# Kernel tuning notes

Measured on AMD Instinct MI355X. Metric: run time of the kernel, lower is better.

The kernel has to match this reference:

```python
import jax, jax.numpy as jnp
import numpy as np

QUERY_LEVELS = jnp.array([300, 500, 900, 1500], dtype=jnp.int32)
MAX_K = 1500
NUM_BOUNDARIES = 3
MAX_OBJECTS = 1500
SCALE = MAX_OBJECTS / NUM_BOUNDARIES * 0.3  # 150.0


def _layernorm(x, g, b, eps=1e-5):
    m = jnp.mean(x, axis=-1, keepdims=True)
    v = jnp.var(x, axis=-1, keepdims=True)
    return (x - m) * jax.lax.rsqrt(v + eps) * g + b


def setup_inputs() -> dict:
    key = jax.random.key(0)
    ks = jax.random.split(key, 14)
    B, C, H, W = 8, 256, 100, 100
    s = 0.02
    return {
        "density_feature": jax.random.normal(ks[0], (B, C, H, W), jnp.float32),
        "encoder_features": jax.random.normal(ks[1], (B, C, H, W), jnp.float32),
        # input_norm (LayerNorm over 2*C)
        "ln_in_g": jnp.ones((2 * C,), jnp.float32),
        "ln_in_b": jnp.zeros((2 * C,), jnp.float32),
        # fc_boundary: Linear(2C->C), Linear(C->3)
        "fcb_w1": jax.random.normal(ks[2], (C, 2 * C), jnp.float32) * s,
        "fcb_b1": jnp.zeros((C,), jnp.float32),
        "fcb_w2": jax.random.normal(ks[3], (NUM_BOUNDARIES, C), jnp.float32) * s,
        "fcb_b2": jnp.full((NUM_BOUNDARIES,), -3.0, jnp.float32),
        "cr_ln_g": jnp.ones((C,), jnp.float32),
        "cr_ln_b": jnp.zeros((C,), jnp.float32),
        "cr_w1": jax.random.normal(ks[4], (C, C), jnp.float32) * s,
        "cr_b1": jnp.zeros((C,), jnp.float32),
        "cr_w2": jax.random.normal(ks[5], (1, C), jnp.float32) * s,
        "cr_b2": jnp.full((1,), 4.0, jnp.float32),
        # channel attention 1x1 convs: C->C//16->C
        "ca_w1": jax.random.normal(ks[6], (C // 16, C), jnp.float32) * s,
        "ca_b1": jnp.zeros((C // 16,), jnp.float32),
        "ca_w2": jax.random.normal(ks[7], (C, C // 16), jnp.float32) * s,
        "ca_b2": jnp.zeros((C,), jnp.float32),
        # spatial attention 7x7 conv, 2->1, no bias
        "sa_w": jax.random.normal(ks[8], (1, 2, 7, 7), jnp.float32) * s,
        # spatial_weight_conv 1x1, C->1
        "sw_w": jax.random.normal(ks[9], (1, C), jnp.float32) * s,
        "sw_b": jnp.zeros((1,), jnp.float32),
    }


def reference(density_feature, encoder_features, ln_in_g, ln_in_b,
              fcb_w1, fcb_b1, fcb_w2, fcb_b2,
              cr_ln_g, cr_ln_b, cr_w1, cr_b1, cr_w2, cr_b2,
              ca_w1, ca_b1, ca_w2, ca_b2, sa_w, sw_w, sw_b):
    B, C, H, W = density_feature.shape
    df = jnp.clip(density_feature, -5.0, 5.0)
    ef = jnp.clip(encoder_features, -5.0, 5.0)

    # ---- boundary prediction from density feature ----
    feat_avg = jnp.mean(df, axis=(2, 3))            # [B, C]
    feat_max = jnp.max(df, axis=(2, 3))             # [B, C]
    gfeat = jnp.concatenate([feat_avg, feat_max], axis=1)  # [B, 2C]
    gfeat = _layernorm(gfeat, ln_in_g, ln_in_b)
    h = jax.nn.relu(gfeat @ fcb_w1.T + fcb_b1)
    raw_boundaries = h @ fcb_w2.T + fcb_b2           # [B, 3]
    # cumulative: b_i = sum_{j<=i} (softplus(raw_j)*SCALE + 5)
    boundaries = jnp.cumsum(jax.nn.softplus(raw_boundaries) * SCALE + 5.0, axis=1)

    cr = _layernorm(feat_avg, cr_ln_g, cr_ln_b)
    cr = jax.nn.relu(cr @ cr_w1.T + cr_b1)
    pred_count = jax.nn.softplus(cr @ cr_w2.T + cr_b2)[:, 0]  # [B]

    # ---- num_queries via boundary comparison (eval: N_eval = pred_count) ----
    level = ((pred_count > boundaries[:, 0]).astype(jnp.int32)
             + (pred_count > boundaries[:, 1]).astype(jnp.int32)
             + (pred_count > boundaries[:, 2]).astype(jnp.int32))
    num_queries = QUERY_LEVELS[level]

    # ---- CBAM channel attention ----
    x = ef
    gap = jnp.mean(x, axis=(2, 3))                   # [B, C]
    ca = jax.nn.relu(gap @ ca_w1.T + ca_b1)
    ca = jax.nn.sigmoid(ca @ ca_w2.T + ca_b2)        # [B, C]
    x = x * ca[:, :, None, None]

    # ---- CBAM spatial attention ----
    sa_avg = jnp.mean(x, axis=1, keepdims=True)      # [B,1,H,W]
    sa_max = jnp.max(x, axis=1, keepdims=True)
    sa = jnp.concatenate([sa_avg, sa_max], axis=1)   # [B,2,H,W]
    sa = jax.lax.conv_general_dilated(sa, sa_w, (1, 1), [(3, 3), (3, 3)],
                                      dimension_numbers=("NCHW", "OIHW", "NCHW"))
    x = x * jax.nn.sigmoid(sa)

    # ---- spatial weight map + topk reference points ----
    wmap = jax.nn.sigmoid(jnp.einsum("bchw,oc->bohw", x, sw_w) + sw_b[None, :, None, None])
    spatial_weight_map = wmap.reshape(B, 1, H * W)
    weight_flat = wmap.reshape(B, H * W)
    actual_k = min(H * W, MAX_K)
    _, topk_ind = jax.lax.top_k(weight_flat, actual_k)   # [B, k]
    topk_y = ((topk_ind // W).astype(jnp.float32) + 0.5) / H
    topk_x = ((topk_ind % W).astype(jnp.float32) + 0.5) / W
    ref_points = jnp.stack([topk_x, topk_y], axis=-1)    # [B,k,2]
    ref_points = jnp.concatenate([ref_points, jnp.full_like(ref_points, 0.05)], axis=-1)
    if actual_k < MAX_K:
        pad = jnp.zeros((B, MAX_K - actual_k, 4), ref_points.dtype)
        ref_points = jnp.concatenate([ref_points, pad], axis=1)

    return (boundaries, raw_boundaries, pred_count, num_queries,
            spatial_weight_map, ref_points)
```

## Files before the change

kernel.cpp:

```cpp
#include <hip/hip_runtime.h>
#include <cstdint>
#include <cstddef>

#define BB 8
#define CC 256
#define HH 100
#define WW 100
#define HW 10000
#define KTOP 1500

#define WS_AVG   0
#define WS_MAX   2048
#define WS_GAP   4096
#define WS_CA    6144
#define WS_CASW  8192
#define WS_SW    10240
#define WS_SAVG  90240
#define WS_SMAX  170240
#define WS_SEL   250240
#define WS_AK    250248

#define O_BND 0
#define O_RAW 24
#define O_CNT 48
#define O_NQ  56
#define O_WMAP 64
#define O_REF 80064

__device__ __forceinline__ float clip5(float v){ return fminf(fmaxf(v, -5.f), 5.f); }
__device__ __forceinline__ float softplusf(float x){ return fmaxf(x, 0.f) + log1pf(expf(-fabsf(x))); }
__device__ __forceinline__ float sigmoidf(float x){ return 1.f / (1.f + expf(-x)); }

__device__ __forceinline__ float wsum(float v){
#pragma unroll
  for (int o = 32; o; o >>= 1) v += __shfl_down(v, o, 64);
  return v;
}
__device__ __forceinline__ float wmaxr(float v){
#pragma unroll
  for (int o = 32; o; o >>= 1) v = fmaxf(v, __shfl_down(v, o, 64));
  return v;
}

__device__ __forceinline__ float bsum256(float v, volatile float* red){
  v = wsum(v);
  int w = threadIdx.x >> 6;
  if ((threadIdx.x & 63) == 0) red[w] = v;
  __syncthreads();
  float r = (red[0] + red[1]) + (red[2] + red[3]);
  __syncthreads();
  return r;
}

__global__ __launch_bounds__(256) void k_reduce(const float* __restrict__ df,
                                                const float* __restrict__ ef,
                                                float* __restrict__ ws){
  int blk = blockIdx.x;
  bool isDf = blk < 2048;
  int bc = isDf ? blk : blk - 2048;
  const float4* __restrict__ src =
      reinterpret_cast<const float4*>((isDf ? df : ef) + (size_t)bc * HW);
  int t = threadIdx.x;
  bool tail = t < (2500 - 9 * 256);
  float4 v[9];
#pragma unroll
  for (int k = 0; k < 9; k++) v[k] = src[t + 256 * k];
  float4 v9 = src[tail ? (2304 + t) : t];

  float s = 0.f, m = -1e30f;
#pragma unroll
  for (int k = 0; k < 9; k++){
    float a = clip5(v[k].x), b = clip5(v[k].y), c = clip5(v[k].z), d = clip5(v[k].w);
    s += (a + b) + (c + d);
    m = fmaxf(m, fmaxf(fmaxf(a, b), fmaxf(c, d)));
  }
  if (tail){
    float a = clip5(v9.x), b = clip5(v9.y), c = clip5(v9.z), d = clip5(v9.w);
    s += (a + b) + (c + d);
    m = fmaxf(m, fmaxf(fmaxf(a, b), fmaxf(c, d)));
  }

  __shared__ float rs[4], rm[4];
  s = wsum(s); m = wmaxr(m);
  int w = t >> 6;
  if ((t & 63) == 0){ rs[w] = s; rm[w] = m; }
  __syncthreads();
  if (t == 0){
    float S = (rs[0] + rs[1]) + (rs[2] + rs[3]);
    float M = fmaxf(fmaxf(rm[0], rm[1]), fmaxf(rm[2], rm[3]));
    if (isDf){ ws[WS_AVG + bc] = S * (1.f / HW); ws[WS_MAX + bc] = M; }
    else      { ws[WS_GAP + bc] = S * (1.f / HW); }
  }
}

__global__ __launch_bounds__(256) void k_head(float* __restrict__ ws,
    const float* __restrict__ ln_g, const float* __restrict__ ln_b,
    const float* __restrict__ fw1, const float* __restrict__ fb1,
    const float* __restrict__ fw2, const float* __restrict__ fb2,
    const float* __restrict__ crg, const float* __restrict__ crb,
    const float* __restrict__ cw1, const float* __restrict__ cb1,
    const float* __restrict__ cw2, const float* __restrict__ cb2,
    const float* __restrict__ caw1, const float* __restrict__ cab1,
    const float* __restrict__ caw2, const float* __restrict__ cab2,
    const float* __restrict__ sw_w, float* __restrict__ out){
  int b = blockIdx.x, t = threadIdx.x;
  __shared__ float red[4];
  __shared__ __align__(16) float gl[512];
  __shared__ __align__(16) float hl[256];
  __shared__ float rawl[3];
  __shared__ float bnd[3];
  __shared__ __align__(16) float al[16];

  float fa = ws[WS_AVG + b * CC + t];
  float fm = ws[WS_MAX + b * CC + t];

  float s  = bsum256(fa + fm, red);
  float s2 = bsum256(fa * fa + fm * fm, red);
  float mean = s * (1.f / 512.f);
  float var  = s2 * (1.f / 512.f) - mean * mean;
  float inv  = rsqrtf(var + 1e-5f);
  gl[t]       = (fa - mean) * inv * ln_g[t]       + ln_b[t];
  gl[t + 256] = (fm - mean) * inv * ln_g[t + 256] + ln_b[t + 256];
  __syncthreads();

  {
    const float4* __restrict__ glv = reinterpret_cast<const float4*>(gl);
    const float4* __restrict__ w1v = reinterpret_cast<const float4*>(fw1 + t * 512);
    float acc = fb1[t];
#pragma unroll 8
    for (int k = 0; k < 128; k++){
      float4 g = glv[k], w = w1v[k];
      acc += g.x * w.x + g.y * w.y + g.z * w.z + g.w * w.w;
    }
    hl[t] = fmaxf(acc, 0.f);
  }
  __syncthreads();
  if (t < 3){
    const float4* __restrict__ hv  = reinterpret_cast<const float4*>(hl);
    const float4* __restrict__ w2v = reinterpret_cast<const float4*>(fw2 + t * 256);
    float r = fb2[t];
#pragma unroll 8
    for (int k = 0; k < 64; k++){
      float4 h = hv[k], w = w2v[k];
      r += h.x * w.x + h.y * w.y + h.z * w.z + h.w * w.w;
    }
    rawl[t] = r;
  }
  __syncthreads();
  if (t == 0){
    float cum = 0.f;
    for (int o = 0; o < 3; o++){
      float rv = rawl[o];
      out[O_RAW + b * 3 + o] = rv;
      cum += softplusf(rv) * 150.f + 5.f;
      out[O_BND + b * 3 + o] = cum;
      bnd[o] = cum;
    }
  }
  __syncthreads();

  float sc  = bsum256(fa, red);
  float sc2 = bsum256(fa * fa, red);
  float m2 = sc * (1.f / 256.f);
  float v2 = sc2 * (1.f / 256.f) - m2 * m2;
  float inv2 = rsqrtf(v2 + 1e-5f);
  hl[t] = (fa - m2) * inv2 * crg[t] + crb[t];
  __syncthreads();
  float h2;
  {
    const float4* __restrict__ hv  = reinterpret_cast<const float4*>(hl);
    const float4* __restrict__ w1v = reinterpret_cast<const float4*>(cw1 + t * 256);
    float acc2 = cb1[t];
#pragma unroll 8
    for (int k = 0; k < 64; k++){
      float4 h = hv[k], w = w1v[k];
      acc2 += h.x * w.x + h.y * w.y + h.z * w.z + h.w * w.w;
    }
    h2 = fmaxf(acc2, 0.f);
  }
  float pv = bsum256(h2 * cw2[t], red);
  if (t == 0){
    float pred = softplusf(pv + cb2[0]);
    out[O_CNT + b] = pred;
    int lvl = (pred > bnd[0]) + (pred > bnd[1]) + (pred > bnd[2]);
    const float QL[4] = {300.f, 500.f, 900.f, 1500.f};
    out[O_NQ + b] = QL[lvl];
  }

  float gp = ws[WS_GAP + b * CC + t];
  __syncthreads();
  hl[t] = gp;
  __syncthreads();
  if (t < 16){
    const float4* __restrict__ hv  = reinterpret_cast<const float4*>(hl);
    const float4* __restrict__ w1v = reinterpret_cast<const float4*>(caw1 + t * 256);
    float a = cab1[t];
#pragma unroll 8
    for (int k = 0; k < 64; k++){
      float4 h = hv[k], w = w1v[k];
      a += h.x * w.x + h.y * w.y + h.z * w.z + h.w * w.w;
    }
    al[t] = fmaxf(a, 0.f);
  }
  __syncthreads();
  float a2 = cab2[t];
  {
    const float4* __restrict__ av  = reinterpret_cast<const float4*>(al);
    const float4* __restrict__ w2v = reinterpret_cast<const float4*>(caw2 + t * 16);
#pragma unroll
    for (int k = 0; k < 4; k++){
      float4 h = av[k], w = w2v[k];
      a2 += h.x * w.x + h.y * w.y + h.z * w.z + h.w * w.w;
    }
  }
  float cav = sigmoidf(a2);
  ws[WS_CA + b * CC + t]   = cav;
  ws[WS_CASW + b * CC + t] = cav * sw_w[t];
}

__global__ __launch_bounds__(128) void k_pixel(const float* __restrict__ ef,
                                               float* __restrict__ ws){
  int b = blockIdx.y;
  int q = blockIdx.x * 128 + threadIdx.x;
  __shared__ float caL[256], cswL[256];
  caL[threadIdx.x]        = ws[WS_CA + b * CC + threadIdx.x];
  caL[threadIdx.x + 128]  = ws[WS_CA + b * CC + threadIdx.x + 128];
  cswL[threadIdx.x]       = ws[WS_CASW + b * CC + threadIdx.x];
  cswL[threadIdx.x + 128] = ws[WS_CASW + b * CC + threadIdx.x + 128];
  __syncthreads();
  if (q >= HW / 4) return;
  const float4* __restrict__ base =
      reinterpret_cast<const float4*>(ef + (size_t)b * CC * HW) + q;
  float4 sum = {0.f, 0.f, 0.f, 0.f};
  float4 mx  = {-1e30f, -1e30f, -1e30f, -1e30f};
  float4 sw  = {0.f, 0.f, 0.f, 0.f};
#pragma unroll 8
  for (int c = 0; c < CC; c++){
    float4 v = base[(size_t)c * (HW / 4)];
    float ca = caL[c], cs = cswL[c];
    float a = clip5(v.x), bb2 = clip5(v.y), cc2 = clip5(v.z), dd = clip5(v.w);
    sum.x += a * ca;  sum.y += bb2 * ca;  sum.z += cc2 * ca;  sum.w += dd * ca;
    mx.x = fmaxf(mx.x, a * ca);  mx.y = fmaxf(mx.y, bb2 * ca);
    mx.z = fmaxf(mx.z, cc2 * ca); mx.w = fmaxf(mx.w, dd * ca);
    sw.x = fmaf(a, cs, sw.x);  sw.y = fmaf(bb2, cs, sw.y);
    sw.z = fmaf(cc2, cs, sw.z); sw.w = fmaf(dd, cs, sw.w);
  }
  float4 avg = {sum.x * (1.f / 256.f), sum.y * (1.f / 256.f),
                sum.z * (1.f / 256.f), sum.w * (1.f / 256.f)};
  reinterpret_cast<float4*>(ws + WS_SAVG + (size_t)b * HW)[q] = avg;
  reinterpret_cast<float4*>(ws + WS_SMAX + (size_t)b * HW)[q] = mx;
  reinterpret_cast<float4*>(ws + WS_SW   + (size_t)b * HW)[q] = sw;
}

__global__ __launch_bounds__(256) void k_conv(const float* __restrict__ ws,
                                              const float* __restrict__ sa_w,
                                              const float* __restrict__ sw_b,
                                              float* __restrict__ out){
  __shared__ float wc[98];
  if (threadIdx.x < 98) wc[threadIdx.x] = sa_w[threadIdx.x];
  __syncthreads();
  int b = blockIdx.y;
  int p = blockIdx.x * 256 + threadIdx.x;
  if (p >= HW) return;
  int h = p / WW, w = p - h * WW;
  const float* s0 = ws + WS_SAVG + (size_t)b * HW;
  const float* s1 = ws + WS_SMAX + (size_t)b * HW;
  float acc = 0.f;
#pragma unroll
  for (int kh = 0; kh < 7; kh++){
    int hy = h + kh - 3;
    if (hy < 0 || hy >= HH) continue;
#pragma unroll
    for (int kw = 0; kw < 7; kw++){
      int wx = w + kw - 3;
      if (wx < 0 || wx >= WW) continue;
      int q = hy * WW + wx;
      acc += s0[q] * wc[kh * 7 + kw] + s1[q] * wc[49 + kh * 7 + kw];
    }
  }
  float wm = sigmoidf(ws[WS_SW + (size_t)b * HW + p] * sigmoidf(acc) + sw_b[0]);
  out[O_WMAP + (size_t)b * HW + p] = wm;
}

__global__ __launch_bounds__(1024) void k_select(const float* __restrict__ outw,
                                                 float* __restrict__ ws,
                                                 float* __restrict__ out){
  __shared__ unsigned long long red64[16];
  __shared__ unsigned red32[16];
  __shared__ unsigned slo, shi, sbc;
  __shared__ unsigned acnt, runbase;
  int b = blockIdx.x, t = threadIdx.x;
  int w = t >> 6, lane = t & 63;

  const float* src = outw + O_WMAP + (size_t)b * HW;
  unsigned rv[10];
#pragma unroll
  for (int j = 0; j < 10; j++){
    int i = t + j * 1024;
    rv[j] = (i < HW) ? __float_as_uint(src[i]) : 0u;
  }

  unsigned lo = 0u, hi = 0xFFFFFFFFu;
  while (lo < hi){
    unsigned span = hi - lo;
    unsigned q1 = lo + (span >> 2);
    unsigned q2 = lo + (span >> 1);
    unsigned q3 = lo + span - (span >> 2);
    unsigned long long pk = 0;
#pragma unroll
    for (int j = 0; j < 10; j++){
      unsigned v = rv[j];
      pk += (unsigned long long)(v > q1)
          + ((unsigned long long)(v > q2) << 16)
          + ((unsigned long long)(v > q3) << 32);
    }
#pragma unroll
    for (int o = 32; o; o >>= 1) pk += __shfl_down(pk, o, 64);
    if (lane == 0) red64[w] = pk;
    __syncthreads();
    if (t == 0){
      unsigned long long tot = 0;
#pragma unroll
      for (int q = 0; q < 16; q++) tot += red64[q];
      unsigned c1 = (unsigned)(tot & 0xFFFFu);
      unsigned c2 = (unsigned)((tot >> 16) & 0xFFFFu);
      unsigned c3 = (unsigned)((tot >> 32) & 0xFFFFu);
      unsigned nlo, nhi;
      if (c1 < (unsigned)KTOP)      { nlo = lo;      nhi = q1; }
      else if (c2 < (unsigned)KTOP) { nlo = q1 + 1u; nhi = q2; }
      else if (c3 < (unsigned)KTOP) { nlo = q2 + 1u; nhi = q3; }
      else                          { nlo = q3 + 1u; nhi = hi; }
      slo = nlo; shi = nhi;
    }
    __syncthreads();
    lo = slo; hi = shi;
    __syncthreads();
  }
  unsigned vthr = lo;

  {
    unsigned c = 0;
#pragma unroll
    for (int j = 0; j < 10; j++) c += (rv[j] > vthr) ? 1u : 0u;
#pragma unroll
    for (int o = 32; o; o >>= 1) c += __shfl_down((int)c, o, 64);
    if (lane == 0) red32[w] = c;
    __syncthreads();
    if (t == 0){
      unsigned tot = 0;
#pragma unroll
      for (int q = 0; q < 16; q++) tot += red32[q];
      sbc = tot;
      acnt = 0; runbase = 0;
    }
    __syncthreads();
  }
  unsigned nabove = sbc;
  int neq = KTOP - (int)nabove;
  if (t == 0) reinterpret_cast<int*>(ws)[WS_SEL + b] = (int)nabove;

  unsigned long long* AK = reinterpret_cast<unsigned long long*>(ws + WS_AK) + (size_t)b * KTOP;
#pragma unroll
  for (int j = 0; j < 10; j++){
    int i = t + j * 1024;
    bool p = (i < HW) && (rv[j] > vthr);
    unsigned long long m = __ballot(p);
    unsigned base = 0;
    if (lane == 0 && m) base = atomicAdd(&acnt, (unsigned)__popcll(m));
    base = (unsigned)__shfl((int)base, 0, 64);
    if (p){
      unsigned pos = base + (unsigned)__popcll(m & ((1ull << lane) - 1ull));
      AK[pos] = ((unsigned long long)rv[j] << 32) | (unsigned long long)(0xFFFFFFFFu - (unsigned)i);
    }
  }

  for (int j = 0; j < 10; j++){
    int i = j * 1024 + t;
    bool eq = (i < HW) && (rv[j] == vthr);
    unsigned long long bal = __ballot(eq);
    if (lane == 0) red32[w] = (unsigned)__popcll(bal);
    __syncthreads();
    unsigned pre = runbase;
    for (int q = 0; q < w; q++) pre += red32[q];
    unsigned myr = pre + (unsigned)__popcll(bal & ((1ull << lane) - 1ull));
    if (eq && myr < (unsigned)neq){
      int pos = (int)nabove + (int)myr;
      float y = ((float)(i / WW) + 0.5f) * (1.f / HH);
      float x = ((float)(i % WW) + 0.5f) * (1.f / WW);
      float* rp = out + O_REF + ((size_t)b * KTOP + pos) * 4;
      rp[0] = x; rp[1] = y; rp[2] = 0.05f; rp[3] = 0.05f;
    }
    __syncthreads();
    if (t == 0){
      unsigned tot = 0;
#pragma unroll
      for (int q = 0; q < 16; q++) tot += red32[q];
      runbase += tot;
    }
    __syncthreads();
    if (runbase >= (unsigned)neq) break;
  }
}

__global__ __launch_bounds__(128) void k_rank(const float* __restrict__ ws,
                                              float* __restrict__ out){
  int b = blockIdx.x, chunk = blockIdx.y, t = threadIdx.x;
  int nA = reinterpret_cast<const int*>(ws)[WS_SEL + b];
  __shared__ unsigned long long K[KTOP];
  const unsigned long long* AK =
      reinterpret_cast<const unsigned long long*>(ws + WS_AK) + (size_t)b * KTOP;
  for (int i = t; i < nA; i += 128) K[i] = AK[i];
  __syncthreads();
  int i = chunk * 128 + t;
  if (i >= nA) return;
  unsigned long long Ki = K[i];
  int r = 0;
  for (int j = 0; j < nA; j++) r += (K[j] > Ki);
  unsigned idx = 0xFFFFFFFFu - (unsigned)(Ki & 0xFFFFFFFFull);
  float y = ((float)(idx / WW) + 0.5f) * (1.f / HH);
  float x = ((float)(idx % WW) + 0.5f) * (1.f / WW);
  float* rp = out + O_REF + ((size_t)b * KTOP + r) * 4;
  rp[0] = x; rp[1] = y; rp[2] = 0.05f; rp[3] = 0.05f;
}

extern "C" void kernel_launch(void* const* d_in, const int* in_sizes, int n_in,
                              void* d_out, int out_size, void* d_ws, size_t ws_size,
                              hipStream_t stream) {
  const float* df   = (const float*)d_in[0];
  const float* ef   = (const float*)d_in[1];
  const float* ln_g = (const float*)d_in[2];
  const float* ln_b = (const float*)d_in[3];
  const float* fw1  = (const float*)d_in[4];
  const float* fb1  = (const float*)d_in[5];
  const float* fw2  = (const float*)d_in[6];
  const float* fb2  = (const float*)d_in[7];
  const float* crg  = (const float*)d_in[8];
  const float* crb  = (const float*)d_in[9];
  const float* cw1  = (const float*)d_in[10];
  const float* cb1  = (const float*)d_in[11];
  const float* cw2  = (const float*)d_in[12];
  const float* cb2  = (const float*)d_in[13];
  const float* caw1 = (const float*)d_in[14];
  const float* cab1 = (const float*)d_in[15];
  const float* caw2 = (const float*)d_in[16];
  const float* cab2 = (const float*)d_in[17];
  const float* sa_w = (const float*)d_in[18];
  const float* sw_w = (const float*)d_in[19];
  const float* sw_b = (const float*)d_in[20];
  float* out = (float*)d_out;
  float* ws  = (float*)d_ws;

  k_reduce<<<4096, 256, 0, stream>>>(df, ef, ws);
  k_head<<<8, 256, 0, stream>>>(ws, ln_g, ln_b, fw1, fb1, fw2, fb2,
                                crg, crb, cw1, cb1, cw2, cb2,
                                caw1, cab1, caw2, cab2, sw_w, out);
  k_pixel<<<dim3(20, 8), 128, 0, stream>>>(ef, ws);
  k_conv<<<dim3(40, 8), 256, 0, stream>>>(ws, sa_w, sw_b, out);
  k_select<<<8, 1024, 0, stream>>>(out, ws, out);
  k_rank<<<dim3(8, 12), 128, 0, stream>>>(ws, out);
}
```

Baseline: 168.6 us.

## Split k_pixel channel loop across waves with double-buffered loads and LDS reduction

```diff
diff --git a/kernel.cpp b/kernel.cpp
--- a/kernel.cpp
+++ b/kernel.cpp
@@ -8,6 +8,7 @@
 #define WW 100
 #define HW 10000
 #define KTOP 1500
+#define QB 64
 
 #define WS_AVG   0
 #define WS_MAX   2048
@@ -61,11 +62,13 @@
   const float4* __restrict__ src =
       reinterpret_cast<const float4*>((isDf ? df : ef) + (size_t)bc * HW);
   int t = threadIdx.x;
-  bool tail = t < (2500 - 9 * 256);
-  float4 v[9];
-#pragma unroll
-  for (int k = 0; k < 9; k++) v[k] = src[t + 256 * k];
-  float4 v9 = src[tail ? (2304 + t) : t];
+  float4 v[10];
+#pragma unroll
+  for (int k = 0; k < 10; k++){
+    int idx = t + 256 * k;
+    v[k] = src[idx < 2500 ? idx : (idx - 2500)];
+  }
+  __builtin_amdgcn_sched_barrier(0);
 
   float s = 0.f, m = -1e30f;
 #pragma unroll
@@ -74,8 +77,8 @@
     s += (a + b) + (c + d);
     m = fmaxf(m, fmaxf(fmaxf(a, b), fmaxf(c, d)));
   }
-  if (tail){
-    float a = clip5(v9.x), b = clip5(v9.y), c = clip5(v9.z), d = clip5(v9.w);
+  if (t < (2500 - 9 * 256)){
+    float a = clip5(v[9].x), b = clip5(v[9].y), c = clip5(v[9].z), d = clip5(v[9].w);
     s += (a + b) + (c + d);
     m = fmaxf(m, fmaxf(fmaxf(a, b), fmaxf(c, d)));
   }
@@ -218,38 +221,81 @@
   ws[WS_CASW + b * CC + t] = cav * sw_w[t];
 }
 
-__global__ __launch_bounds__(128) void k_pixel(const float* __restrict__ ef,
+__device__ __forceinline__ void px_acc(const float4& v, float ca, float cs,
+                                       float4& sum, float4& mx, float4& sw){
+  float a = clip5(v.x), b = clip5(v.y), c = clip5(v.z), d = clip5(v.w);
+  sum.x += a * ca; sum.y += b * ca; sum.z += c * ca; sum.w += d * ca;
+  mx.x = fmaxf(mx.x, a * ca); mx.y = fmaxf(mx.y, b * ca);
+  mx.z = fmaxf(mx.z, c * ca); mx.w = fmaxf(mx.w, d * ca);
+  sw.x = fmaf(a, cs, sw.x); sw.y = fmaf(b, cs, sw.y);
+  sw.z = fmaf(c, cs, sw.z); sw.w = fmaf(d, cs, sw.w);
+}
+
+__global__ __launch_bounds__(256) void k_pixel(const float* __restrict__ ef,
                                                float* __restrict__ ws){
   int b = blockIdx.y;
-  int q = blockIdx.x * 128 + threadIdx.x;
+  int t = threadIdx.x;
+  int w = t >> 6, lane = t & 63;
   __shared__ float caL[256], cswL[256];
-  caL[threadIdx.x]        = ws[WS_CA + b * CC + threadIdx.x];
-  caL[threadIdx.x + 128]  = ws[WS_CA + b * CC + threadIdx.x + 128];
-  cswL[threadIdx.x]       = ws[WS_CASW + b * CC + threadIdx.x];
-  cswL[threadIdx.x + 128] = ws[WS_CASW + b * CC + threadIdx.x + 128];
-  __syncthreads();
-  if (q >= HW / 4) return;
+  __shared__ float4 part[3][4][QB];
+  caL[t]  = ws[WS_CA + b * CC + t];
+  cswL[t] = ws[WS_CASW + b * CC + t];
+  __syncthreads();
+
+  int q = blockIdx.x * QB + lane;
+  const size_t st = HW / 4;
+  size_t off = (q < (int)st) ? (size_t)q : 0;
   const float4* __restrict__ base =
-      reinterpret_cast<const float4*>(ef + (size_t)b * CC * HW) + q;
+      reinterpret_cast<const float4*>(ef + (size_t)b * CC * HW) + off;
+  int c0 = w * 64;
+
   float4 sum = {0.f, 0.f, 0.f, 0.f};
   float4 mx  = {-1e30f, -1e30f, -1e30f, -1e30f};
   float4 sw  = {0.f, 0.f, 0.f, 0.f};
-#pragma unroll 8
-  for (int c = 0; c < CC; c++){
-    float4 v = base[(size_t)c * (HW / 4)];
-    float ca = caL[c], cs = cswL[c];
-    float a = clip5(v.x), bb2 = clip5(v.y), cc2 = clip5(v.z), dd = clip5(v.w);
-    sum.x += a * ca;  sum.y += bb2 * ca;  sum.z += cc2 * ca;  sum.w += dd * ca;
-    mx.x = fmaxf(mx.x, a * ca);  mx.y = fmaxf(mx.y, bb2 * ca);
-    mx.z = fmaxf(mx.z, cc2 * ca); mx.w = fmaxf(mx.w, dd * ca);
-    sw.x = fmaf(a, cs, sw.x);  sw.y = fmaf(bb2, cs, sw.y);
-    sw.z = fmaf(cc2, cs, sw.z); sw.w = fmaf(dd, cs, sw.w);
-  }
-  float4 avg = {sum.x * (1.f / 256.f), sum.y * (1.f / 256.f),
-                sum.z * (1.f / 256.f), sum.w * (1.f / 256.f)};
-  reinterpret_cast<float4*>(ws + WS_SAVG + (size_t)b * HW)[q] = avg;
-  reinterpret_cast<float4*>(ws + WS_SMAX + (size_t)b * HW)[q] = mx;
-  reinterpret_cast<float4*>(ws + WS_SW   + (size_t)b * HW)[q] = sw;
+
+  float4 A[8], Bv[8];
+#pragma unroll
+  for (int j = 0; j < 8; j++) A[j] = base[(size_t)(c0 + j) * st];
+#pragma unroll
+  for (int s = 0; s < 4; s++){
+    int cA = c0 + (2 * s) * 8;
+    int cB = c0 + (2 * s + 1) * 8;
+#pragma unroll
+    for (int j = 0; j < 8; j++) Bv[j] = base[(size_t)(cB + j) * st];
+#pragma unroll
+    for (int j = 0; j < 8; j++) px_acc(A[j], caL[cA + j], cswL[cA + j], sum, mx, sw);
+    if (s < 3){
+      int cN = c0 + (2 * s + 2) * 8;
+#pragma unroll
+      for (int j = 0; j < 8; j++) A[j] = base[(size_t)(cN + j) * st];
+    }
+#pragma unroll
+    for (int j = 0; j < 8; j++) px_acc(Bv[j], caL[cB + j], cswL[cB + j], sum, mx, sw);
+  }
+
+  part[0][w][lane] = sum;
+  part[1][w][lane] = mx;
+  part[2][w][lane] = sw;
+  __syncthreads();
+  if (t < QB){
+    float4 S = part[0][0][t], M = part[1][0][t], W4 = part[2][0][t];
+#pragma unroll
+    for (int wv = 1; wv < 4; wv++){
+      float4 s1 = part[0][wv][t], m1 = part[1][wv][t], w1 = part[2][wv][t];
+      S.x += s1.x; S.y += s1.y; S.z += s1.z; S.w += s1.w;
+      M.x = fmaxf(M.x, m1.x); M.y = fmaxf(M.y, m1.y);
+      M.z = fmaxf(M.z, m1.z); M.w = fmaxf(M.w, m1.w);
+      W4.x += w1.x; W4.y += w1.y; W4.z += w1.z; W4.w += w1.w;
+    }
+    int q2 = blockIdx.x * QB + t;
+    if (q2 < (int)st){
+      float4 avg = {S.x * (1.f / 256.f), S.y * (1.f / 256.f),
+                    S.z * (1.f / 256.f), S.w * (1.f / 256.f)};
+      reinterpret_cast<float4*>(ws + WS_SAVG + (size_t)b * HW)[q2] = avg;
+      reinterpret_cast<float4*>(ws + WS_SMAX + (size_t)b * HW)[q2] = M;
+      reinterpret_cast<float4*>(ws + WS_SW   + (size_t)b * HW)[q2] = W4;
+    }
+  }
 }
 
 __global__ __launch_bounds__(256) void k_conv(const float* __restrict__ ws,
@@ -454,7 +500,7 @@
   k_head<<<8, 256, 0, stream>>>(ws, ln_g, ln_b, fw1, fb1, fw2, fb2,
                                 crg, crb, cw1, cb1, cw2, cb2,
                                 caw1, cab1, caw2, cab2, sw_w, out);
-  k_pixel<<<dim3(20, 8), 128, 0, stream>>>(ef, ws);
+  k_pixel<<<dim3(40, 8), 256, 0, stream>>>(ef, ws);
   k_conv<<<dim3(40, 8), 256, 0, stream>>>(ws, sa_w, sw_b, out);
   k_select<<<8, 1024, 0, stream>>>(out, ws, out);
   k_rank<<<dim3(8, 12), 128, 0, stream>>>(ws, out);
```

Result: faster. 146.7 us (-13.0%).
